# Performance work log

Hardware: AMD Instinct MI355X
Metric: run time of the kernel (lower is better)

Reference implementation:

```python
import jax, jax.numpy as jnp
import numpy as np
import math

B, N, D_MODEL = 1, 2925, 1536
NUM_HEADS, HEAD_DIM = 12, 128
F, H, W = 13, 15, 15
MAX_SEQ = 1024
EPS = 1e-6


def _make_freqs(max_seq, dim):
    # (cos, sin) pairs for half-dim rotary frequencies, base 10000
    inv = 1.0 / (10000.0 ** (np.arange(0, dim, 2, dtype=np.float64) / dim))
    ang = np.arange(max_seq, dtype=np.float64)[:, None] * inv[None, :]
    return jnp.asarray(np.stack([np.cos(ang), np.sin(ang)], axis=-1), dtype=jnp.float32)


def setup_inputs() -> dict:
    key = jax.random.key(0)
    ks = jax.random.split(key, 10)
    s = 1.0 / math.sqrt(D_MODEL)
    dim_base = HEAD_DIM // 6              # 21
    dim_t = HEAD_DIM - 4 * dim_base       # 44
    dim_h = 2 * dim_base                  # 42
    return {
        "x": jax.random.normal(ks[0], (B, N, D_MODEL), dtype=jnp.float32),
        "Wq": jax.random.normal(ks[1], (D_MODEL, D_MODEL), dtype=jnp.float32) * s,
        "bq": jnp.zeros((D_MODEL,), dtype=jnp.float32),
        "Wk": jax.random.normal(ks[2], (D_MODEL, D_MODEL), dtype=jnp.float32) * s,
        "bk": jnp.zeros((D_MODEL,), dtype=jnp.float32),
        "Wv": jax.random.normal(ks[3], (D_MODEL, D_MODEL), dtype=jnp.float32) * s,
        "bv": jnp.zeros((D_MODEL,), dtype=jnp.float32),
        "Wo": jax.random.normal(ks[4], (D_MODEL, D_MODEL), dtype=jnp.float32) * s,
        "bo": jnp.zeros((D_MODEL,), dtype=jnp.float32),
        "q_scale": jnp.ones((D_MODEL,), dtype=jnp.float32),
        "k_scale": jnp.ones((D_MODEL,), dtype=jnp.float32),
        "freqs_t": _make_freqs(MAX_SEQ, dim_t),
        "freqs_h": _make_freqs(MAX_SEQ, dim_h),
        "freqs_w": _make_freqs(MAX_SEQ, dim_h),
        "f": F, "h": H, "w": W,
    }


def _rms_norm(x, scale, eps=EPS):
    var = jnp.mean(jnp.square(x), axis=-1, keepdims=True)
    return x * jax.lax.rsqrt(var + eps) * scale


def _rope_apply(x, f, h, w, freqs_t, freqs_h, freqs_w):
    # x: [b, n, H, D] with n == f*h*w
    b, n, nh, d = x.shape
    db = d // 6
    dt, dh, dw = d - 4 * db, 2 * db, 2 * db
    ft = jnp.broadcast_to(freqs_t[:f, None, None, :, :], (f, h, w, dt // 2, 2))
    fh = jnp.broadcast_to(freqs_h[None, :h, None, :, :], (f, h, w, dh // 2, 2))
    fw = jnp.broadcast_to(freqs_w[None, None, :w, :, :], (f, h, w, dw // 2, 2))
    fg = jnp.concatenate([ft, fh, fw], axis=3).reshape(n, d // 2, 2)[None, :, None, :, :]
    xc = x.reshape(b, n, nh, d // 2, 2)
    re = xc[..., 0] * fg[..., 0] - xc[..., 1] * fg[..., 1]
    im = xc[..., 0] * fg[..., 1] + xc[..., 1] * fg[..., 0]
    return jnp.stack([re, im], axis=-1).reshape(b, n, nh, d)


def reference(x, Wq, bq, Wk, bk, Wv, bv, Wo, bo, q_scale, k_scale,
              freqs_t, freqs_h, freqs_w, f, h, w):
    b, n, _ = x.shape
    nh, d = NUM_HEADS, HEAD_DIM
    # projections + RMSNorm across full hidden dim (before head split)
    q = _rms_norm(x @ Wq + bq, q_scale).reshape(b, n, nh, d)
    k = _rms_norm(x @ Wk + bk, k_scale).reshape(b, n, nh, d)
    v = (x @ Wv + bv).reshape(b, n, nh, d)
    # 3D RoPE on [b, n, H, D] layout
    q = _rope_apply(q, f, h, w, freqs_t, freqs_h, freqs_w)
    k = _rope_apply(k, f, h, w, freqs_t, freqs_h, freqs_w)
    # [b, H, n, d]
    q = q.transpose(0, 2, 1, 3)
    k = k.transpose(0, 2, 1, 3)
    v = v.transpose(0, 2, 1, 3)
    scores = jnp.einsum("bhid,bhjd->bhij", q, k) / math.sqrt(d)
    attn = jax.nn.softmax(scores, axis=-1)
    out = jnp.einsum("bhij,bhjd->bhid", attn, v)
    out = out.transpose(0, 2, 1, 3).reshape(b, n, nh * d)
    return out @ Wo + bo
```

## Files before the change

kernel.cpp:

```cpp
#include <hip/hip_runtime.h>


#define N_TOK 2925
#define DMODEL 1536
#define NHEAD 12
#define HDIM 128
#define KSPLIT 1472
#define VT_STRIDE 2944

typedef __attribute__((ext_vector_type(8))) __bf16 bf16x8;
typedef __attribute__((ext_vector_type(4))) float floatx4;

#define MFMA(a, b, c) __builtin_amdgcn_mfma_f32_16x16x32_bf16((a), (b), (c), 0, 0, 0)

static __device__ __forceinline__ unsigned short f2bf(float f) {
    unsigned u = __builtin_bit_cast(unsigned, f);
    return (unsigned short)((u + 0x7fffu + ((u >> 16) & 1u)) >> 16);
}

static __device__ __forceinline__ void gload_lds16(const unsigned short* g, unsigned short* l) {
    __builtin_amdgcn_global_load_lds((const __attribute__((address_space(1))) void*)g,
                                     (__attribute__((address_space(3))) void*)l, 16, 0, 0);
}

__global__ __launch_bounds__(256) void k_convert_x(const float* __restrict__ x,
                                                   unsigned short* __restrict__ xb, int n) {
    int i = (blockIdx.x * 256 + threadIdx.x) * 4;
    if (i < n) {
        float4 v = *(const float4*)(x + i);
        uint2 o;
        o.x = (unsigned)f2bf(v.x) | ((unsigned)f2bf(v.y) << 16);
        o.y = (unsigned)f2bf(v.z) | ((unsigned)f2bf(v.w) << 16);
        *(uint2*)(xb + i) = o;
    }
}

__global__ __launch_bounds__(256) void k_transpose_w(const float* __restrict__ W0,
                                                     const float* __restrict__ W1,
                                                     const float* __restrict__ W2,
                                                     const float* __restrict__ W3,
                                                     unsigned short* __restrict__ Wt) {
    __shared__ float tile[32][33];
    const float* W = blockIdx.z == 0 ? W0 : blockIdx.z == 1 ? W1 : blockIdx.z == 2 ? W2 : W3;
    unsigned short* out = Wt + (size_t)blockIdx.z * DMODEL * DMODEL;
    int tx = threadIdx.x, ty = threadIdx.y;
    int bx = blockIdx.x * 32, by = blockIdx.y * 32;
#pragma unroll
    for (int i = 0; i < 4; i++)
        tile[ty + 8 * i][tx] = W[(size_t)(by + ty + 8 * i) * DMODEL + bx + tx];
    __syncthreads();
#pragma unroll
    for (int i = 0; i < 4; i++)
        out[(size_t)(bx + ty + 8 * i) * DMODEL + by + tx] = f2bf(tile[tx][ty + 8 * i]);
}

__global__ __launch_bounds__(512, 2) void k_gemm_qkv(const unsigned short* __restrict__ A,
                                                     const unsigned short* __restrict__ BtBase,
                                                     const float* __restrict__ b0,
                                                     const float* __restrict__ b1,
                                                     const float* __restrict__ b2,
                                                     float* __restrict__ Cbase, int M) {
    __shared__ __align__(16) unsigned short As[2][256 * 64];
    __shared__ __align__(16) unsigned short Bs[2][256 * 64];

    const int blin = blockIdx.x + 6 * (blockIdx.y + 12 * (int)blockIdx.z);
    const int wg = (blin & 7) * 27 + (blin >> 3);
    const int z = wg / 72, rem = wg % 72, mt = rem / 6, ntile = rem % 6;
    const unsigned short* Bt = BtBase + (size_t)z * DMODEL * DMODEL;
    const float* bias = (z == 0) ? b0 : (z == 1) ? b1 : b2;
    float* C = Cbase + (size_t)z * M * DMODEL;
    const int m0 = mt * 256, n0 = ntile * 256;

    const int tid = threadIdx.x;
    const int wave = tid >> 6, lane = tid & 63, quad = lane >> 4, l16 = lane & 15;
    const int x7 = l16 & 7;
    const int wm = wave >> 2, wn = wave & 3;

    const int koff0 = ((quad) ^ x7) * 8;
    const int koff1 = ((4 + quad) ^ x7) * 8;

    const int sl = tid & 7;

    floatx4 acc[8][4] = {};

    const unsigned short* Abase = A + (size_t)m0 * DMODEL;
    const unsigned short* Bbase = Bt + (size_t)n0 * DMODEL;

    auto stageB = [&](int buf, int h, int kt) {
#pragma unroll
        for (int i = 0; i < 2; i++) {
            int d = tid + 512 * i;
            int row = h * 128 + (d >> 3);
            int c = sl ^ (row & 7);
            gload_lds16(Bbase + (size_t)row * DMODEL + kt * 64 + c * 8,
                        &Bs[buf][(row * 8 + sl) * 8]);
        }
    };
    auto stageA = [&](int buf, int h, int kt) {
#pragma unroll
        for (int i = 0; i < 2; i++) {
            int d = tid + 512 * i;
            int r7 = d >> 3;
            int row = (r7 & 63) + h * 64 + (r7 >> 6) * 128;
            int c = sl ^ (row & 7);
            gload_lds16(Abase + (size_t)row * DMODEL + kt * 64 + c * 8,
                        &As[buf][(row * 8 + sl) * 8]);
        }
    };

    stageB(0, 0, 0); stageB(0, 1, 0); stageA(0, 0, 0); stageA(0, 1, 0);

    const int NT = DMODEL / 64;
    for (int t = 0; t < NT; t++) {
        const int c = t & 1, sb = c ^ 1;
        const int ts = (t + 1 < NT) ? t + 1 : NT - 1;

        asm volatile("s_waitcnt vmcnt(2)" ::: "memory");
        __builtin_amdgcn_sched_barrier(0);
        __builtin_amdgcn_s_barrier();

        bf16x8 af[4], bfm[4];
#pragma unroll
        for (int m = 0; m < 4; m++)
            af[m] = *(const bf16x8*)&As[c][(wm * 128 + m * 16 + l16) * 64 + koff0];
#pragma unroll
        for (int n = 0; n < 4; n++)
            bfm[n] = *(const bf16x8*)&Bs[c][(wn * 64 + n * 16 + l16) * 64 + koff0];
        stageB(sb, 0, ts);
        __builtin_amdgcn_s_barrier();
        __builtin_amdgcn_s_setprio(1);
#pragma unroll
        for (int m = 0; m < 4; m++)
#pragma unroll
            for (int n = 0; n < 4; n++)
                acc[m][n] = MFMA(af[m], bfm[n], acc[m][n]);
        __builtin_amdgcn_s_setprio(0);
        __builtin_amdgcn_sched_barrier(0);

        asm volatile("s_waitcnt vmcnt(2)" ::: "memory");
        __builtin_amdgcn_sched_barrier(0);
        __builtin_amdgcn_s_barrier();

        bf16x8 af2[4];
#pragma unroll
        for (int m = 0; m < 4; m++)
            af2[m] = *(const bf16x8*)&As[c][(wm * 128 + 64 + m * 16 + l16) * 64 + koff0];
        stageB(sb, 1, ts);
        __builtin_amdgcn_s_barrier();
        __builtin_amdgcn_s_setprio(1);
#pragma unroll
        for (int m = 0; m < 4; m++)
#pragma unroll
            for (int n = 0; n < 4; n++)
                acc[4 + m][n] = MFMA(af2[m], bfm[n], acc[4 + m][n]);
        __builtin_amdgcn_s_setprio(0);
        __builtin_amdgcn_sched_barrier(0);

#pragma unroll
        for (int m = 0; m < 4; m++)
            af[m] = *(const bf16x8*)&As[c][(wm * 128 + m * 16 + l16) * 64 + koff1];
#pragma unroll
        for (int n = 0; n < 4; n++)
            bfm[n] = *(const bf16x8*)&Bs[c][(wn * 64 + n * 16 + l16) * 64 + koff1];
        stageA(sb, 0, ts);
        __builtin_amdgcn_s_barrier();
        __builtin_amdgcn_s_setprio(1);
#pragma unroll
        for (int m = 0; m < 4; m++)
#pragma unroll
            for (int n = 0; n < 4; n++)
                acc[m][n] = MFMA(af[m], bfm[n], acc[m][n]);
        __builtin_amdgcn_s_setprio(0);
        __builtin_amdgcn_sched_barrier(0);

#pragma unroll
        for (int m = 0; m < 4; m++)
            af2[m] = *(const bf16x8*)&As[c][(wm * 128 + 64 + m * 16 + l16) * 64 + koff1];
        stageA(sb, 1, ts);
        __builtin_amdgcn_s_barrier();
        __builtin_amdgcn_s_setprio(1);
#pragma unroll
        for (int m = 0; m < 4; m++)
#pragma unroll
            for (int n = 0; n < 4; n++)
                acc[4 + m][n] = MFMA(af2[m], bfm[n], acc[4 + m][n]);
        __builtin_amdgcn_s_setprio(0);
        __builtin_amdgcn_sched_barrier(0);
    }

#pragma unroll
    for (int n = 0; n < 4; n++) {
        int cg = n0 + wn * 64 + n * 16 + l16;
        float bv = bias[cg];
#pragma unroll
        for (int m = 0; m < 8; m++) {
            int rbase = m0 + wm * 128 + m * 16 + quad * 4;
#pragma unroll
            for (int r = 0; r < 4; r++) {
                int rg = rbase + r;
                if (rg < M) C[(size_t)rg * DMODEL + cg] = acc[m][n][r] + bv;
            }
        }
    }
}

__global__ __launch_bounds__(256, 3) void k_gemm(const unsigned short* __restrict__ A,
                                                 const unsigned short* __restrict__ BtBase,
                                                 const float* __restrict__ b0,
                                                 const float* __restrict__ b1,
                                                 const float* __restrict__ b2,
                                                 float* __restrict__ Cbase, int M) {
    const int nbx = gridDim.x, nxy = gridDim.x * gridDim.y;
    const int nb = nxy * gridDim.z;
    const int blin = blockIdx.x + nbx * (blockIdx.y + gridDim.y * blockIdx.z);
    const int q8 = nb >> 3, r8 = nb & 7, xcd = blin & 7, idx = blin >> 3;
    const int wg = (xcd < r8) ? xcd * (q8 + 1) + idx
                              : r8 * (q8 + 1) + (xcd - r8) * q8 + idx;
    const int z = wg / nxy;
    const int rem = wg % nxy;
    const int bym = rem / nbx, bxn = rem % nbx;

    const unsigned short* Bt = BtBase + (size_t)z * DMODEL * DMODEL;
    const float* bias = (z == 0) ? b0 : (z == 1) ? b1 : b2;
    float* C = Cbase + (size_t)z * M * DMODEL;

    __shared__ __align__(16) unsigned short As[128 * 32];
    __shared__ __align__(16) unsigned short Bs[128 * 32];

    const int tid = threadIdx.x;
    const int wave = tid >> 6, lane = tid & 63, quad = lane >> 4, l16 = lane & 15;
    const int wr = wave >> 1, wc = wave & 1;
    const int m0 = bym * 128, n0 = bxn * 128;
    const int r4 = tid >> 2, c4 = (tid & 3) * 8;

    floatx4 acc[4][4] = {};

    for (int k0 = 0; k0 < DMODEL; k0 += 32) {
        gload_lds16(A + (size_t)(m0 + r4) * DMODEL + k0 + c4,       &As[r4 * 32 + c4]);
        gload_lds16(A + (size_t)(m0 + r4 + 64) * DMODEL + k0 + c4,  &As[(r4 + 64) * 32 + c4]);
        gload_lds16(Bt + (size_t)(n0 + r4) * DMODEL + k0 + c4,      &Bs[r4 * 32 + c4]);
        gload_lds16(Bt + (size_t)(n0 + r4 + 64) * DMODEL + k0 + c4, &Bs[(r4 + 64) * 32 + c4]);
        __syncthreads();

        bf16x8 af[4], bfm[4];
#pragma unroll
        for (int i = 0; i < 4; i++)
            af[i] = *(const bf16x8*)&As[(wr * 64 + i * 16 + l16) * 32 + quad * 8];
#pragma unroll
        for (int j = 0; j < 4; j++)
            bfm[j] = *(const bf16x8*)&Bs[(wc * 64 + j * 16 + l16) * 32 + quad * 8];
#pragma unroll
        for (int i = 0; i < 4; i++)
#pragma unroll
            for (int j = 0; j < 4; j++)
                acc[i][j] = MFMA(af[i], bfm[j], acc[i][j]);
        __syncthreads();
    }

#pragma unroll
    for (int j = 0; j < 4; j++) {
        int cg = n0 + wc * 64 + j * 16 + l16;
        float bv = bias[cg];
#pragma unroll
        for (int i = 0; i < 4; i++) {
            int rbase = m0 + wr * 64 + i * 16 + quad * 4;
#pragma unroll
            for (int r = 0; r < 4; r++) {
                int rg = rbase + r;
                if (rg < M) C[(size_t)rg * DMODEL + cg] = acc[i][j][r] + bv;
            }
        }
    }
}

__global__ __launch_bounds__(256) void k_norm_rope(const float* __restrict__ Qf,
                                                   const float* __restrict__ Kf,
                                                   const float* __restrict__ Vf,
                                                   const float* __restrict__ qsc,
                                                   const float* __restrict__ ksc,
                                                   const float* __restrict__ ft,
                                                   const float* __restrict__ fh,
                                                   const float* __restrict__ fw,
                                                   unsigned short* __restrict__ qb,
                                                   unsigned short* __restrict__ kb,
                                                   unsigned short* __restrict__ vb) {
    const int n = blockIdx.x;
    const int tid = threadIdx.x, wave = tid >> 6, lane = tid & 63;
    const int t_i = n / 225, rem = n % 225, h_i = rem / 15, w_i = rem % 15;
    const float att_scale = 0.08838834764831845f * 1.4426950408889634f;

    float2 qv[3], kv[3], vv[3];
    float sq = 0.f, sk = 0.f;
#pragma unroll
    for (int c = 0; c < 3; c++) {
        int p = tid + 256 * c;
        qv[c] = *(const float2*)(Qf + (size_t)n * DMODEL + 2 * p);
        kv[c] = *(const float2*)(Kf + (size_t)n * DMODEL + 2 * p);
        vv[c] = *(const float2*)(Vf + (size_t)n * DMODEL + 2 * p);
        sq += qv[c].x * qv[c].x + qv[c].y * qv[c].y;
        sk += kv[c].x * kv[c].x + kv[c].y * kv[c].y;
    }
#pragma unroll
    for (int off = 32; off >= 1; off >>= 1) {
        sq += __shfl_xor(sq, off, 64);
        sk += __shfl_xor(sk, off, 64);
    }
    __shared__ float red[2][4];
    if (lane == 0) { red[0][wave] = sq; red[1][wave] = sk; }
    __syncthreads();
    sq = red[0][0] + red[0][1] + red[0][2] + red[0][3];
    sk = red[1][0] + red[1][1] + red[1][2] + red[1][3];
    const float rq = rsqrtf(sq * (1.f / 1536.f) + 1e-6f) * att_scale;
    const float rk = rsqrtf(sk * (1.f / 1536.f) + 1e-6f);

#pragma unroll
    for (int c = 0; c < 3; c++) {
        int p = tid + 256 * c;
        int hd = p >> 6, pl = p & 63, dd = 2 * pl;
        float cs, sn;
        if (pl < 22)      { cs = ft[t_i * 44 + 2 * pl];        sn = ft[t_i * 44 + 2 * pl + 1]; }
        else if (pl < 43) { int pp = pl - 22; cs = fh[h_i * 42 + 2 * pp]; sn = fh[h_i * 42 + 2 * pp + 1]; }
        else              { int pp = pl - 43; cs = fw[w_i * 42 + 2 * pp]; sn = fw[w_i * 42 + 2 * pp + 1]; }
        int hidx = hd * 128 + dd;
        float q0 = qv[c].x * rq * qsc[hidx], q1 = qv[c].y * rq * qsc[hidx + 1];
        float k0 = kv[c].x * rk * ksc[hidx], k1 = kv[c].y * rk * ksc[hidx + 1];
        size_t o = ((size_t)hd * N_TOK + n) * HDIM + dd;
        unsigned qo = (unsigned)f2bf(q0 * cs - q1 * sn) | ((unsigned)f2bf(q0 * sn + q1 * cs) << 16);
        unsigned ko = (unsigned)f2bf(k0 * cs - k1 * sn) | ((unsigned)f2bf(k0 * sn + k1 * cs) << 16);
        unsigned vo = (unsigned)f2bf(vv[c].x) | ((unsigned)f2bf(vv[c].y) << 16);
        *(unsigned*)(qb + o) = qo;
        *(unsigned*)(kb + o) = ko;
        *(unsigned*)(vb + o) = vo;
    }
}

__global__ __launch_bounds__(256) void k_transpose_v(const unsigned short* __restrict__ vbi,
                                                     unsigned short* __restrict__ vt) {
    __shared__ unsigned short tile[32][33];
    const int head = blockIdx.z;
    const int t0 = blockIdx.x * 32, d0 = blockIdx.y * 32;
    const int tx = threadIdx.x, ty = threadIdx.y;
#pragma unroll
    for (int i = 0; i < 4; i++) {
        int t = t0 + ty + 8 * i;
        tile[ty + 8 * i][tx] = (t < N_TOK) ? vbi[((size_t)head * N_TOK + t) * HDIM + d0 + tx] : 0;
    }
    __syncthreads();
    int t = t0 + tx;
#pragma unroll
    for (int i = 0; i < 4; i++)
        vt[((size_t)head * HDIM + d0 + ty + 8 * i) * VT_STRIDE + t] = tile[tx][ty + 8 * i];
}

__global__ __launch_bounds__(256, 4) void k_attn_part(const unsigned short* __restrict__ qb,
                                                      const unsigned short* __restrict__ kb,
                                                      const unsigned short* __restrict__ vt,
                                                      float* __restrict__ Opart,
                                                      float* __restrict__ mbuf,
                                                      float* __restrict__ lbuf) {
    __shared__ __align__(16) unsigned short Ks[64 * 128];
    __shared__ __align__(16) unsigned short Vs[128 * 64];
    __shared__ __align__(16) unsigned short Ps[4][16 * 64];

    const int b = blockIdx.x + 46 * (blockIdx.y + 12 * (int)blockIdx.z);
    const int w = (b & 7) * 138 + (b >> 3);
    const int qblk = w % 46;
    const int head = (w / 46) % 12;
    const int z    = w / 552;

    const int tid = threadIdx.x, wave = tid >> 6, lane = tid & 63;
    const int quad = lane >> 4, l16 = lane & 15, x7 = l16 & 7;
    const int q0 = qblk * 64 + wave * 16;
    const unsigned short* qh = qb + (size_t)head * N_TOK * HDIM;
    const unsigned short* kh = kb + (size_t)head * N_TOK * HDIM;
    const unsigned short* vh = vt + (size_t)head * HDIM * VT_STRIDE;
    unsigned short* ps = Ps[wave];

    const int kbeg = z ? KSPLIT : 0;
    const int kend = z ? N_TOK : KSPLIT;
    const int ntile = (kend - kbeg + 63) >> 6;

    int koff[4];
#pragma unroll
    for (int ks = 0; ks < 4; ks++) {
        int c = ks * 4 + quad;
        koff[ks] = ((c & 8) | ((c & 7) ^ x7)) * 8;
    }
    const int pwq = (quad >> 1), pwh = (quad & 1) * 4;

    const int krow = tid >> 4, ksw = tid & 15;
    const int kc = (ksw & 8) | ((ksw & 7) ^ (krow & 7));
    const int vd = tid >> 3, vsw = tid & 7;
    const int vc = vsw ^ (vd & 7);
    const unsigned short* ksrc = kh + (size_t)krow * HDIM + kc * 8;
    const unsigned short* vsrc = vh + (size_t)vd * VT_STRIDE + vc * 8;

    bf16x8 aq[4];
    {
        int qrow = q0 + l16;
        if (qrow < N_TOK) {
#pragma unroll
            for (int ks = 0; ks < 4; ks++)
                aq[ks] = *(const bf16x8*)&qh[(size_t)qrow * HDIM + ks * 32 + quad * 8];
        } else {
#pragma unroll
            for (int ks = 0; ks < 4; ks++) aq[ks] = (bf16x8)(__bf16)0.0f;
        }
    }

    floatx4 oacc[8] = {};
    float m_l = -1e30f;
    float l_l = 0.f;

    {
        const bool part0 = (kbeg + 64 > kend);
        if (!part0) {
#pragma unroll
            for (int i = 0; i < 4; i++)
                gload_lds16(ksrc + (size_t)(kbeg + 16 * i) * HDIM, &Ks[(tid + 256 * i) * 8]);
        } else {
#pragma unroll
            for (int i = 0; i < 4; i++) {
                int gk = kbeg + krow + 16 * i;
                gk = gk < N_TOK ? gk : N_TOK - 1;
                gload_lds16(kh + (size_t)gk * HDIM + kc * 8, &Ks[(tid + 256 * i) * 8]);
            }
        }
#pragma unroll
        for (int i = 0; i < 4; i++)
            gload_lds16(vsrc + (size_t)(32 * i) * VT_STRIDE + kbeg, &Vs[(tid + 256 * i) * 8]);
    }

    for (int t = 0; t < ntile; t++) {
        const int kb0 = kbeg + t * 64;
        const bool fullt = (kb0 + 64 <= kend);
        const bool has_next = (t + 1 < ntile);

        asm volatile("s_waitcnt vmcnt(4)" ::: "memory");
        __builtin_amdgcn_sched_barrier(0);
        __builtin_amdgcn_s_barrier();

        floatx4 sa[4] = {};
        __builtin_amdgcn_s_setprio(1);
#pragma unroll
        for (int j = 0; j < 4; j++)
#pragma unroll
            for (int ks = 0; ks < 4; ks++) {
                bf16x8 bkf = *(const bf16x8*)&Ks[(j * 16 + l16) * HDIM + koff[ks]];
                sa[j] = MFMA(bkf, aq[ks], sa[j]);
            }
        __builtin_amdgcn_s_setprio(0);
        __builtin_amdgcn_s_barrier();

        if (has_next) {
            const int kn = kb0 + 64;
            if (kn + 64 <= kend) {
#pragma unroll
                for (int i = 0; i < 4; i++)
                    gload_lds16(ksrc + (size_t)(kn + 16 * i) * HDIM, &Ks[(tid + 256 * i) * 8]);
            } else {
#pragma unroll
                for (int i = 0; i < 4; i++) {
                    int gk = kn + krow + 16 * i;
                    gk = gk < N_TOK ? gk : N_TOK - 1;
                    gload_lds16(kh + (size_t)gk * HDIM + kc * 8, &Ks[(tid + 256 * i) * 8]);
                }
            }
        }

        float mt;
        if (fullt) {
            float m01 = fmaxf(fmaxf(sa[0][0], sa[0][1]), fmaxf(sa[0][2], sa[0][3]));
            float m23 = fmaxf(fmaxf(sa[1][0], sa[1][1]), fmaxf(sa[1][2], sa[1][3]));
            float m45 = fmaxf(fmaxf(sa[2][0], sa[2][1]), fmaxf(sa[2][2], sa[2][3]));
            float m67 = fmaxf(fmaxf(sa[3][0], sa[3][1]), fmaxf(sa[3][2], sa[3][3]));
            mt = fmaxf(fmaxf(m01, m23), fmaxf(m45, m67));
        } else {
            mt = -1e30f;
            const int kq = kb0 + quad * 4;
#pragma unroll
            for (int j = 0; j < 4; j++)
#pragma unroll
                for (int r = 0; r < 4; r++)
                    mt = fmaxf(mt, (kq + j * 16 + r < kend) ? sa[j][r] : -1e30f);
        }
        mt = fmaxf(mt, __shfl_xor(mt, 16));
        mt = fmaxf(mt, __shfl_xor(mt, 32));

        if (__any(mt > m_l + 8.f)) {
            float mn = fmaxf(m_l, mt);
            float alpha = exp2f(m_l - mn);
            m_l = mn;
            l_l *= alpha;
#pragma unroll
            for (int r = 0; r < 4; r++) {
                float ar = __shfl(alpha, quad * 4 + r, 16);
#pragma unroll
                for (int jd = 0; jd < 8; jd++) oacc[jd][r] *= ar;
            }
        }

        if (fullt) {
#pragma unroll
            for (int j = 0; j < 4; j++) {
                float p0 = exp2f(sa[j][0] - m_l), p1 = exp2f(sa[j][1] - m_l);
                float p2 = exp2f(sa[j][2] - m_l), p3 = exp2f(sa[j][3] - m_l);
                l_l += (p0 + p1) + (p2 + p3);
                uint2 wv;
                wv.x = (unsigned)__builtin_bit_cast(unsigned short, (__bf16)p0) |
                       ((unsigned)__builtin_bit_cast(unsigned short, (__bf16)p1) << 16);
                wv.y = (unsigned)__builtin_bit_cast(unsigned short, (__bf16)p2) |
                       ((unsigned)__builtin_bit_cast(unsigned short, (__bf16)p3) << 16);
                *(uint2*)&ps[l16 * 64 + (((j * 2 + pwq) ^ x7) << 3) + pwh] = wv;
            }
        } else {
            const int kq = kb0 + quad * 4;
#pragma unroll
            for (int j = 0; j < 4; j++) {
                float p[4];
#pragma unroll
                for (int r = 0; r < 4; r++) {
                    p[r] = (kq + j * 16 + r < kend) ? exp2f(sa[j][r] - m_l) : 0.f;
                    l_l += p[r];
                }
                uint2 wv;
                wv.x = (unsigned)__builtin_bit_cast(unsigned short, (__bf16)p[0]) |
                       ((unsigned)__builtin_bit_cast(unsigned short, (__bf16)p[1]) << 16);
                wv.y = (unsigned)__builtin_bit_cast(unsigned short, (__bf16)p[2]) |
                       ((unsigned)__builtin_bit_cast(unsigned short, (__bf16)p[3]) << 16);
                *(uint2*)&ps[l16 * 64 + (((j * 2 + pwq) ^ x7) << 3) + pwh] = wv;
            }
        }

        if (has_next) { asm volatile("s_waitcnt vmcnt(4)" ::: "memory"); }
        else          { asm volatile("s_waitcnt vmcnt(0)" ::: "memory"); }
        __builtin_amdgcn_sched_barrier(0);
        __builtin_amdgcn_s_barrier();

        __builtin_amdgcn_s_setprio(1);
#pragma unroll
        for (int ks = 0; ks < 2; ks++) {
            bf16x8 ap = *(const bf16x8*)&ps[l16 * 64 + koff[ks]];
#pragma unroll
            for (int jd = 0; jd < 8; jd++) {
                bf16x8 bvf = *(const bf16x8*)&Vs[(jd * 16 + l16) * 64 + koff[ks]];
                oacc[jd] = MFMA(ap, bvf, oacc[jd]);
            }
        }
        __builtin_amdgcn_s_setprio(0);
        __builtin_amdgcn_s_barrier();

        if (has_next) {
            const int kn = kb0 + 64;
#pragma unroll
            for (int i = 0; i < 4; i++)
                gload_lds16(vsrc + (size_t)(32 * i) * VT_STRIDE + kn, &Vs[(tid + 256 * i) * 8]);
        }
    }

    l_l += __shfl_xor(l_l, 16);
    l_l += __shfl_xor(l_l, 32);

#pragma unroll
    for (int r = 0; r < 4; r++) {
        int rg = q0 + quad * 4 + r;
        if (rg < N_TOK) {
            size_t rbase = ((size_t)(z * NHEAD + head) * N_TOK + rg) * HDIM;
#pragma unroll
            for (int jd = 0; jd < 8; jd++)
                Opart[rbase + jd * 16 + l16] = oacc[jd][r];
        }
    }
    if (quad == 0 && q0 + l16 < N_TOK) {
        int mi = (z * NHEAD + head) * N_TOK + q0 + l16;
        mbuf[mi] = m_l;
        lbuf[mi] = l_l;
    }
}

__global__ __launch_bounds__(256) void k_combine(const float* __restrict__ Opart,
                                                 const float* __restrict__ mbuf,
                                                 const float* __restrict__ lbuf,
                                                 unsigned short* __restrict__ ab) {
    const int R = NHEAD * N_TOK;
    int r = blockIdx.x * 8 + (threadIdx.x >> 5);
    if (r >= R) return;
    int l32 = threadIdx.x & 31;
    float m0 = mbuf[r], m1 = mbuf[R + r];
    float l0 = lbuf[r], l1 = lbuf[R + r];
    float m = fmaxf(m0, m1);
    float w0 = exp2f(m0 - m), w1 = exp2f(m1 - m);
    float inv = 1.f / (l0 * w0 + l1 * w1);
    w0 *= inv; w1 *= inv;
    float4 a = *(const float4*)&Opart[(size_t)r * HDIM + l32 * 4];
    float4 b = *(const float4*)&Opart[((size_t)R + r) * HDIM + l32 * 4];
    int head = r / N_TOK, tok = r % N_TOK;
    unsigned short* o = ab + (size_t)tok * DMODEL + head * HDIM + l32 * 4;
    uint2 pk;
    pk.x = (unsigned)f2bf(a.x * w0 + b.x * w1) | ((unsigned)f2bf(a.y * w0 + b.y * w1) << 16);
    pk.y = (unsigned)f2bf(a.z * w0 + b.z * w1) | ((unsigned)f2bf(a.w * w0 + b.w * w1) << 16);
    *(uint2*)o = pk;
}

extern "C" void kernel_launch(void* const* d_in, const int* in_sizes, int n_in,
                              void* d_out, int out_size, void* d_ws, size_t ws_size,
                              hipStream_t stream) {
    const float* x   = (const float*)d_in[0];
    const float* Wq  = (const float*)d_in[1];
    const float* bq  = (const float*)d_in[2];
    const float* Wk  = (const float*)d_in[3];
    const float* bk  = (const float*)d_in[4];
    const float* Wv  = (const float*)d_in[5];
    const float* bv  = (const float*)d_in[6];
    const float* Wo  = (const float*)d_in[7];
    const float* bo  = (const float*)d_in[8];
    const float* qsc = (const float*)d_in[9];
    const float* ksc = (const float*)d_in[10];
    const float* ft  = (const float*)d_in[11];
    const float* fh  = (const float*)d_in[12];
    const float* fw  = (const float*)d_in[13];

    char* ws = (char*)d_ws;
    unsigned short* xb   = (unsigned short*)ws; ws += (size_t)N_TOK * DMODEL * 2;
    unsigned short* Wt   = (unsigned short*)ws; ws += (size_t)4 * DMODEL * DMODEL * 2;
    unsigned short* ab   = (unsigned short*)ws; ws += (size_t)N_TOK * DMODEL * 2;
    char* qkvf_region    = ws;                  ws += (size_t)3 * N_TOK * DMODEL * 4;
    unsigned short* qkvb = (unsigned short*)ws; ws += (size_t)3 * N_TOK * DMODEL * 2;

    float* Qf = (float*)qkvf_region;
    float* Kf = Qf + (size_t)N_TOK * DMODEL;
    float* Vf = Qf + (size_t)2 * N_TOK * DMODEL;
    float* Opart = (float*)qkvf_region;
    float* mbuf  = Opart + (size_t)2 * NHEAD * N_TOK * HDIM;
    float* lbuf  = mbuf + (size_t)2 * NHEAD * N_TOK;
    unsigned short* vtp = (unsigned short*)(lbuf + (size_t)2 * NHEAD * N_TOK);

    unsigned short* qbp = qkvb;
    unsigned short* kbp = qkvb + (size_t)N_TOK * DMODEL;
    unsigned short* vbp = qkvb + (size_t)2 * N_TOK * DMODEL;

    const int nelem = N_TOK * DMODEL;
    k_convert_x<<<(nelem / 4 + 255) / 256, 256, 0, stream>>>(x, xb, nelem);
    k_transpose_w<<<dim3(48, 48, 4), dim3(32, 8), 0, stream>>>(Wq, Wk, Wv, Wo, Wt);
    k_gemm_qkv<<<dim3(6, 12, 3), 512, 0, stream>>>(xb, Wt, bq, bk, bv, Qf, N_TOK);
    k_norm_rope<<<N_TOK, 256, 0, stream>>>(Qf, Kf, Vf, qsc, ksc, ft, fh, fw, qbp, kbp, vbp);
    k_transpose_v<<<dim3(92, 4, NHEAD), dim3(32, 8), 0, stream>>>(vbp, vtp);
    k_attn_part<<<dim3(46, NHEAD, 2), 256, 0, stream>>>(qbp, kbp, vtp, Opart, mbuf, lbuf);
    k_combine<<<(NHEAD * N_TOK + 7) / 8, 256, 0, stream>>>(Opart, mbuf, lbuf, ab);
    k_gemm<<<dim3(12, 23, 1), 256, 0, stream>>>(ab, Wt + (size_t)3 * DMODEL * DMODEL,
                                                bo, bo, bo, (float*)d_out, N_TOK);
}
```

Before: 355.6 us.

## Drop split-K attention and combine kernel; transpose V straight from fp32

Attention no longer splits the key range in two. Each block processes all keys, normalises by the row sum in the epilogue and writes bf16 output directly into the Wo GEMM input, so the fp32 partial outputs, the m/l buffers and the combine kernel are removed. The V bf16 conversion moves out of the norm/RoPE kernel into the transpose kernel, which now reads fp32 V directly, saving one intermediate write and read. The cost is half as many attention blocks, each running twice as long, which lowers occupancy and latency hiding on the GPU.

```diff
diff --git a/kernel.cpp b/kernel.cpp
--- a/kernel.cpp
+++ b/kernel.cpp
@@ -5,7 +5,6 @@
 #define DMODEL 1536
 #define NHEAD 12
 #define HDIM 128
-#define KSPLIT 1472
 #define VT_STRIDE 2944
 
 typedef __attribute__((ext_vector_type(8))) __bf16 bf16x8;
@@ -78,7 +77,6 @@
 
     const int koff0 = ((quad) ^ x7) * 8;
     const int koff1 = ((4 + quad) ^ x7) * 8;
-
     const int sl = tid & 7;
 
     floatx4 acc[8][4] = {};
@@ -275,28 +273,25 @@
 
 __global__ __launch_bounds__(256) void k_norm_rope(const float* __restrict__ Qf,
                                                    const float* __restrict__ Kf,
-                                                   const float* __restrict__ Vf,
                                                    const float* __restrict__ qsc,
                                                    const float* __restrict__ ksc,
                                                    const float* __restrict__ ft,
                                                    const float* __restrict__ fh,
                                                    const float* __restrict__ fw,
                                                    unsigned short* __restrict__ qb,
-                                                   unsigned short* __restrict__ kb,
-                                                   unsigned short* __restrict__ vb) {
+                                                   unsigned short* __restrict__ kb) {
     const int n = blockIdx.x;
     const int tid = threadIdx.x, wave = tid >> 6, lane = tid & 63;
     const int t_i = n / 225, rem = n % 225, h_i = rem / 15, w_i = rem % 15;
     const float att_scale = 0.08838834764831845f * 1.4426950408889634f;
 
-    float2 qv[3], kv[3], vv[3];
+    float2 qv[3], kv[3];
     float sq = 0.f, sk = 0.f;
 #pragma unroll
     for (int c = 0; c < 3; c++) {
         int p = tid + 256 * c;
         qv[c] = *(const float2*)(Qf + (size_t)n * DMODEL + 2 * p);
         kv[c] = *(const float2*)(Kf + (size_t)n * DMODEL + 2 * p);
-        vv[c] = *(const float2*)(Vf + (size_t)n * DMODEL + 2 * p);
         sq += qv[c].x * qv[c].x + qv[c].y * qv[c].y;
         sk += kv[c].x * kv[c].x + kv[c].y * kv[c].y;
     }
@@ -327,46 +322,41 @@
         size_t o = ((size_t)hd * N_TOK + n) * HDIM + dd;
         unsigned qo = (unsigned)f2bf(q0 * cs - q1 * sn) | ((unsigned)f2bf(q0 * sn + q1 * cs) << 16);
         unsigned ko = (unsigned)f2bf(k0 * cs - k1 * sn) | ((unsigned)f2bf(k0 * sn + k1 * cs) << 16);
-        unsigned vo = (unsigned)f2bf(vv[c].x) | ((unsigned)f2bf(vv[c].y) << 16);
         *(unsigned*)(qb + o) = qo;
         *(unsigned*)(kb + o) = ko;
-        *(unsigned*)(vb + o) = vo;
-    }
-}
-
-__global__ __launch_bounds__(256) void k_transpose_v(const unsigned short* __restrict__ vbi,
-                                                     unsigned short* __restrict__ vt) {
-    __shared__ unsigned short tile[32][33];
+    }
+}
+
+__global__ __launch_bounds__(256) void k_transpose_vf(const float* __restrict__ Vf,
+                                                      unsigned short* __restrict__ vt) {
+    __shared__ float tile[32][33];
     const int head = blockIdx.z;
     const int t0 = blockIdx.x * 32, d0 = blockIdx.y * 32;
     const int tx = threadIdx.x, ty = threadIdx.y;
 #pragma unroll
     for (int i = 0; i < 4; i++) {
         int t = t0 + ty + 8 * i;
-        tile[ty + 8 * i][tx] = (t < N_TOK) ? vbi[((size_t)head * N_TOK + t) * HDIM + d0 + tx] : 0;
+        tile[ty + 8 * i][tx] = (t < N_TOK) ? Vf[(size_t)t * DMODEL + head * HDIM + d0 + tx] : 0.f;
     }
     __syncthreads();
     int t = t0 + tx;
 #pragma unroll
     for (int i = 0; i < 4; i++)
-        vt[((size_t)head * HDIM + d0 + ty + 8 * i) * VT_STRIDE + t] = tile[tx][ty + 8 * i];
+        vt[((size_t)head * HDIM + d0 + ty + 8 * i) * VT_STRIDE + t] = f2bf(tile[tx][ty + 8 * i]);
 }
 
 __global__ __launch_bounds__(256, 4) void k_attn_part(const unsigned short* __restrict__ qb,
                                                       const unsigned short* __restrict__ kb,
                                                       const unsigned short* __restrict__ vt,
-                                                      float* __restrict__ Opart,
-                                                      float* __restrict__ mbuf,
-                                                      float* __restrict__ lbuf) {
+                                                      unsigned short* __restrict__ ab) {
     __shared__ __align__(16) unsigned short Ks[64 * 128];
     __shared__ __align__(16) unsigned short Vs[128 * 64];
     __shared__ __align__(16) unsigned short Ps[4][16 * 64];
 
-    const int b = blockIdx.x + 46 * (blockIdx.y + 12 * (int)blockIdx.z);
-    const int w = (b & 7) * 138 + (b >> 3);
+    const int b = blockIdx.x + 46 * (int)blockIdx.y;
+    const int w = (b & 7) * 69 + (b >> 3);
     const int qblk = w % 46;
-    const int head = (w / 46) % 12;
-    const int z    = w / 552;
+    const int head = w / 46;
 
     const int tid = threadIdx.x, wave = tid >> 6, lane = tid & 63;
     const int quad = lane >> 4, l16 = lane & 15, x7 = l16 & 7;
@@ -376,9 +366,7 @@
     const unsigned short* vh = vt + (size_t)head * HDIM * VT_STRIDE;
     unsigned short* ps = Ps[wave];
 
-    const int kbeg = z ? KSPLIT : 0;
-    const int kend = z ? N_TOK : KSPLIT;
-    const int ntile = (kend - kbeg + 63) >> 6;
+    const int ntile = (N_TOK + 63) >> 6;
 
     int koff[4];
 #pragma unroll
@@ -412,28 +400,16 @@
     float m_l = -1e30f;
     float l_l = 0.f;
 
-    {
-        const bool part0 = (kbeg + 64 > kend);
-        if (!part0) {
-#pragma unroll
-            for (int i = 0; i < 4; i++)
-                gload_lds16(ksrc + (size_t)(kbeg + 16 * i) * HDIM, &Ks[(tid + 256 * i) * 8]);
-        } else {
-#pragma unroll
-            for (int i = 0; i < 4; i++) {
-                int gk = kbeg + krow + 16 * i;
-                gk = gk < N_TOK ? gk : N_TOK - 1;
-                gload_lds16(kh + (size_t)gk * HDIM + kc * 8, &Ks[(tid + 256 * i) * 8]);
-            }
-        }
-#pragma unroll
-        for (int i = 0; i < 4; i++)
-            gload_lds16(vsrc + (size_t)(32 * i) * VT_STRIDE + kbeg, &Vs[(tid + 256 * i) * 8]);
-    }
+#pragma unroll
+    for (int i = 0; i < 4; i++)
+        gload_lds16(ksrc + (size_t)(16 * i) * HDIM, &Ks[(tid + 256 * i) * 8]);
+#pragma unroll
+    for (int i = 0; i < 4; i++)
+        gload_lds16(vsrc + (size_t)(32 * i) * VT_STRIDE, &Vs[(tid + 256 * i) * 8]);
 
     for (int t = 0; t < ntile; t++) {
-        const int kb0 = kbeg + t * 64;
-        const bool fullt = (kb0 + 64 <= kend);
+        const int kb0 = t * 64;
+        const bool fullt = (kb0 + 64 <= N_TOK);
         const bool has_next = (t + 1 < ntile);
 
         asm volatile("s_waitcnt vmcnt(4)" ::: "memory");
@@ -454,7 +430,7 @@
 
         if (has_next) {
             const int kn = kb0 + 64;
-            if (kn + 64 <= kend) {
+            if (kn + 64 <= N_TOK) {
 #pragma unroll
                 for (int i = 0; i < 4; i++)
                     gload_lds16(ksrc + (size_t)(kn + 16 * i) * HDIM, &Ks[(tid + 256 * i) * 8]);
@@ -482,7 +458,7 @@
             for (int j = 0; j < 4; j++)
 #pragma unroll
                 for (int r = 0; r < 4; r++)
-                    mt = fmaxf(mt, (kq + j * 16 + r < kend) ? sa[j][r] : -1e30f);
+                    mt = fmaxf(mt, (kq + j * 16 + r < N_TOK) ? sa[j][r] : -1e30f);
         }
         mt = fmaxf(mt, __shfl_xor(mt, 16));
         mt = fmaxf(mt, __shfl_xor(mt, 32));
@@ -520,7 +496,7 @@
                 float p[4];
 #pragma unroll
                 for (int r = 0; r < 4; r++) {
-                    p[r] = (kq + j * 16 + r < kend) ? exp2f(sa[j][r] - m_l) : 0.f;
+                    p[r] = (kq + j * 16 + r < N_TOK) ? exp2f(sa[j][r] - m_l) : 0.f;
                     l_l += p[r];
                 }
                 uint2 wv;
@@ -560,46 +536,19 @@
 
     l_l += __shfl_xor(l_l, 16);
     l_l += __shfl_xor(l_l, 32);
+    const float inv = 1.f / l_l;
 
 #pragma unroll
     for (int r = 0; r < 4; r++) {
+        const float ir = __shfl(inv, quad * 4 + r, 16);
         int rg = q0 + quad * 4 + r;
         if (rg < N_TOK) {
-            size_t rbase = ((size_t)(z * NHEAD + head) * N_TOK + rg) * HDIM;
+            unsigned short* orow = ab + (size_t)rg * DMODEL + head * HDIM;
 #pragma unroll
             for (int jd = 0; jd < 8; jd++)
-                Opart[rbase + jd * 16 + l16] = oacc[jd][r];
-        }
-    }
-    if (quad == 0 && q0 + l16 < N_TOK) {
-        int mi = (z * NHEAD + head) * N_TOK + q0 + l16;
-        mbuf[mi] = m_l;
-        lbuf[mi] = l_l;
-    }
-}
-
-__global__ __launch_bounds__(256) void k_combine(const float* __restrict__ Opart,
-                                                 const float* __restrict__ mbuf,
-                                                 const float* __restrict__ lbuf,
-                                                 unsigned short* __restrict__ ab) {
-    const int R = NHEAD * N_TOK;
-    int r = blockIdx.x * 8 + (threadIdx.x >> 5);
-    if (r >= R) return;
-    int l32 = threadIdx.x & 31;
-    float m0 = mbuf[r], m1 = mbuf[R + r];
-    float l0 = lbuf[r], l1 = lbuf[R + r];
-    float m = fmaxf(m0, m1);
-    float w0 = exp2f(m0 - m), w1 = exp2f(m1 - m);
-    float inv = 1.f / (l0 * w0 + l1 * w1);
-    w0 *= inv; w1 *= inv;
-    float4 a = *(const float4*)&Opart[(size_t)r * HDIM + l32 * 4];
-    float4 b = *(const float4*)&Opart[((size_t)R + r) * HDIM + l32 * 4];
-    int head = r / N_TOK, tok = r % N_TOK;
-    unsigned short* o = ab + (size_t)tok * DMODEL + head * HDIM + l32 * 4;
-    uint2 pk;
-    pk.x = (unsigned)f2bf(a.x * w0 + b.x * w1) | ((unsigned)f2bf(a.y * w0 + b.y * w1) << 16);
-    pk.y = (unsigned)f2bf(a.z * w0 + b.z * w1) | ((unsigned)f2bf(a.w * w0 + b.w * w1) << 16);
-    *(uint2*)o = pk;
+                orow[jd * 16 + l16] = f2bf(oacc[jd][r] * ir);
+        }
+    }
 }
 
 extern "C" void kernel_launch(void* const* d_in, const int* in_sizes, int n_in,
@@ -625,28 +574,23 @@
     unsigned short* Wt   = (unsigned short*)ws; ws += (size_t)4 * DMODEL * DMODEL * 2;
     unsigned short* ab   = (unsigned short*)ws; ws += (size_t)N_TOK * DMODEL * 2;
     char* qkvf_region    = ws;                  ws += (size_t)3 * N_TOK * DMODEL * 4;
-    unsigned short* qkvb = (unsigned short*)ws; ws += (size_t)3 * N_TOK * DMODEL * 2;
+    unsigned short* qkvb = (unsigned short*)ws; ws += (size_t)2 * N_TOK * DMODEL * 2;
 
     float* Qf = (float*)qkvf_region;
     float* Kf = Qf + (size_t)N_TOK * DMODEL;
     float* Vf = Qf + (size_t)2 * N_TOK * DMODEL;
-    float* Opart = (float*)qkvf_region;
-    float* mbuf  = Opart + (size_t)2 * NHEAD * N_TOK * HDIM;
-    float* lbuf  = mbuf + (size_t)2 * NHEAD * N_TOK;
-    unsigned short* vtp = (unsigned short*)(lbuf + (size_t)2 * NHEAD * N_TOK);
+    unsigned short* vtp = (unsigned short*)qkvf_region;
 
     unsigned short* qbp = qkvb;
     unsigned short* kbp = qkvb + (size_t)N_TOK * DMODEL;
-    unsigned short* vbp = qkvb + (size_t)2 * N_TOK * DMODEL;
 
     const int nelem = N_TOK * DMODEL;
     k_convert_x<<<(nelem / 4 + 255) / 256, 256, 0, stream>>>(x, xb, nelem);
     k_transpose_w<<<dim3(48, 48, 4), dim3(32, 8), 0, stream>>>(Wq, Wk, Wv, Wo, Wt);
     k_gemm_qkv<<<dim3(6, 12, 3), 512, 0, stream>>>(xb, Wt, bq, bk, bv, Qf, N_TOK);
-    k_norm_rope<<<N_TOK, 256, 0, stream>>>(Qf, Kf, Vf, qsc, ksc, ft, fh, fw, qbp, kbp, vbp);
-    k_transpose_v<<<dim3(92, 4, NHEAD), dim3(32, 8), 0, stream>>>(vbp, vtp);
-    k_attn_part<<<dim3(46, NHEAD, 2), 256, 0, stream>>>(qbp, kbp, vtp, Opart, mbuf, lbuf);
-    k_combine<<<(NHEAD * N_TOK + 7) / 8, 256, 0, stream>>>(Opart, mbuf, lbuf, ab);
+    k_norm_rope<<<N_TOK, 256, 0, stream>>>(Qf, Kf, qsc, ksc, ft, fh, fw, qbp, kbp);
+    k_transpose_vf<<<dim3(92, 4, NHEAD), dim3(32, 8), 0, stream>>>(Vf, vtp);
+    k_attn_part<<<dim3(46, NHEAD), 256, 0, stream>>>(qbp, kbp, vtp, ab);
     k_gemm<<<dim3(12, 23, 1), 256, 0, stream>>>(ab, Wt + (size_t)3 * DMODEL * DMODEL,
                                                 bo, bo, bo, (float*)d_out, N_TOK);
 }
```

Result: no change. 352.3 us (-0.9%).
